# Kernel optimization log

Hardware: AMD Instinct MI355X
Metric: run time of the kernel (lower is better)

The kernel has to match this reference:

```python
import jax, jax.numpy as jnp
import numpy as np

N = 50000
E = 800000
IN_C = 128
OUT_C = 64
NEG_SLOPE = 0.2


def setup_inputs() -> dict:
    key = jax.random.key(0)
    k1, k2, k3, k4, k5 = jax.random.split(key, 5)
    x = jax.random.normal(k1, (N, IN_C), dtype=jnp.float32)
    edge_index = jax.random.randint(k2, (2, E), 0, N, dtype=jnp.int64)
    # GATv2Conv params (heads=1): lin_l (source), lin_r (target), att, bias
    sc_in = 1.0 / np.sqrt(IN_C)
    sc_out = 1.0 / np.sqrt(OUT_C)
    W_l = jax.random.normal(k3, (IN_C, OUT_C), dtype=jnp.float32) * sc_in
    W_r = jax.random.normal(k4, (IN_C, OUT_C), dtype=jnp.float32) * sc_in
    att = jax.random.normal(k5, (OUT_C,), dtype=jnp.float32) * sc_out
    bias = jnp.zeros((OUT_C,), dtype=jnp.float32)
    return {"x": x, "edge_index": edge_index, "W_l": W_l, "W_r": W_r,
            "att": att, "bias": bias}


def _gatv2(x, edge_index, W_l, W_r, att, bias):
    n = x.shape[0]
    # add self loops (PyG default add_self_loops=True)
    loop = jnp.arange(n, dtype=edge_index.dtype)
    src = jnp.concatenate([edge_index[0], loop])
    dst = jnpp_concat = jnp.concatenate([edge_index[1], loop])
    x_l = x @ W_l  # source transform [N, C]
    x_r = x @ W_r  # target transform [N, C]
    x_j = x_l[src]                      # [E+N, C] gathered source msgs
    e = jax.nn.leaky_relu(x_j + x_r[dst], NEG_SLOPE)
    logit = e @ att                     # [E+N]
    # segment softmax over edges grouped by destination node
    m = jax.ops.segment_max(logit, dst, num_segments=n)
    m = jnp.where(jnp.isfinite(m), m, 0.0)
    a = jnp.exp(logit - m[dst])
    denom = jax.ops.segment_sum(a, dst, num_segments=n)
    alpha = a / (denom[dst] + 1e-16)
    out = jax.ops.segment_sum(x_j * alpha[:, None], dst, num_segments=n)
    return out + bias


def reference(x, edge_index, W_l, W_r, att, bias):
    # dropout(p=0.6) is identity at inference
    h = jax.nn.elu(_gatv2(x, edge_index, W_l, W_r, att, bias))
    return jax.nn.log_softmax(h, axis=-1)
```

## Files before the change

kernel.cpp:

```cpp
#include <hip/hip_runtime.h>

#define N_NODES 50000
#define N_EDGES 800000
#define IN_C    128
#define OUT_C   64
#define NEG_SLOPE 0.2f

#define CAP     48

#define NB      196
#define NB_PAD  256
#define C_B     5120
#define EPB     4096
#define NP1     ((N_EDGES + EPB - 1) / EPB)
#define G_GEMM  ((N_NODES + 63) / 64)

#define GRID_MEGA 1024

typedef __bf16 bf16_8 __attribute__((ext_vector_type(8)));
typedef float  f32x4  __attribute__((ext_vector_type(4)));

__device__ __forceinline__ unsigned f2bf(float f) {
    unsigned u = __float_as_uint(f);
    return (u + 0x7fffu + ((u >> 16) & 1u)) >> 16;
}

__device__ __forceinline__ void wait_ge(int* ctr, int target) {
    int it = 0;
    while (__hip_atomic_load(ctr, __ATOMIC_ACQUIRE, __HIP_MEMORY_SCOPE_AGENT) < target) {
        __builtin_amdgcn_s_sleep(2);
        if (++it > (1 << 26)) break;
    }
}

__device__ __forceinline__ void grid_barrier(int* ctr, int nblk) {
    __syncthreads();
    if (threadIdx.x == 0) {
        __threadfence();
        __hip_atomic_fetch_add(ctr, 1, __ATOMIC_ACQ_REL, __HIP_MEMORY_SCOPE_AGENT);
        wait_ge(ctr, nblk);
        __threadfence();
    }
    __syncthreads();
}

__global__ __launch_bounds__(256) void k_prep(
    const float* __restrict__ Wl, const float* __restrict__ Wr,
    unsigned short* __restrict__ wtg, int* __restrict__ bcnt)
{
    int i = blockIdx.x * 256 + threadIdx.x;
    int k = i >> 6, cm = i & 63;
    if (k < 128) {
        wtg[(size_t)cm * 128 + k]        = (unsigned short)f2bf(Wl[(size_t)k * 64 + cm]);
        wtg[(size_t)(64 + cm) * 128 + k] = (unsigned short)f2bf(Wr[(size_t)k * 64 + cm]);
    }
    if (i < NB_PAD + 8) bcnt[i] = 0;
}

#define XPAD 136

__global__ __launch_bounds__(256, 4) void k_mega(
    const float* __restrict__ x, const unsigned short* __restrict__ wtg,
    const float* __restrict__ att, const int* __restrict__ ei,
    int* __restrict__ bcnt, unsigned* __restrict__ arena,
    unsigned short* __restrict__ xlb, unsigned short* __restrict__ xrb,
    float* __restrict__ qtil, int* __restrict__ cnt,
    unsigned short* __restrict__ csr_src, const float* __restrict__ bias,
    float* __restrict__ out)
{
    __shared__ __align__(16) char smem[25600];
    const int tid = threadIdx.x;
    const int b = (int)blockIdx.x;
    const int nblk = (int)gridDim.x;
    int* p1done = bcnt + NB_PAD;
    int* fullbar = bcnt + NB_PAD + 1;

    if (b < NP1) {
        unsigned* sorted = (unsigned*)smem;
        int* bc     = (int*)(smem + 16384);
        int* bstart = (int*)(smem + 16384 + 1024);
        int* gbase  = (int*)(smem + 16384 + 2048);
        int* bofs   = (int*)(smem + 16384 + 3072);

        int e0 = b * EPB;
        int nE = N_EDGES - e0; if (nE > EPB) nE = EPB;

        unsigned pk[16]; int bk[16];
#pragma unroll
        for (int jj = 0; jj < 4; ++jj) {
            int rel = jj * 1024 + tid * 4;
            if (rel + 3 < nE) {
                int4 d4 = *(const int4*)(ei + N_EDGES + e0 + rel);
                int4 s4 = *(const int4*)(ei + e0 + rel);
                int d[4] = {d4.x, d4.y, d4.z, d4.w};
                int s[4] = {s4.x, s4.y, s4.z, s4.w};
#pragma unroll
                for (int k2 = 0; k2 < 4; ++k2) {
                    pk[jj*4+k2] = ((unsigned)d[k2] << 16) | (unsigned)s[k2];
                    bk[jj*4+k2] = d[k2] >> 8;
                }
            } else {
#pragma unroll
                for (int k2 = 0; k2 < 4; ++k2) {
                    int e = rel + k2;
                    if (e < nE) {
                        int d = ei[N_EDGES + e0 + e], s = ei[e0 + e];
                        pk[jj*4+k2] = ((unsigned)d << 16) | (unsigned)s;
                        bk[jj*4+k2] = d >> 8;
                    } else bk[jj*4+k2] = -1;
                }
            }
        }

        bc[tid] = 0;
        __syncthreads();
#pragma unroll
        for (int i = 0; i < 16; ++i)
            if (bk[i] >= 0) atomicAdd(&bc[bk[i]], 1);
        __syncthreads();
        if (tid < 64) {
            int c0 = bc[tid*4], c1 = bc[tid*4+1], c2 = bc[tid*4+2], c3 = bc[tid*4+3];
            int t0 = c0, t1 = t0 + c1, t2 = t1 + c2, t3 = t2 + c3;
            int incl = t3;
#pragma unroll
            for (int o = 1; o < 64; o <<= 1) {
                int v = __shfl_up(incl, o);
                if (tid >= o) incl += v;
            }
            int ex = incl - t3;
            bstart[tid*4]   = ex;
            bstart[tid*4+1] = ex + t0;
            bstart[tid*4+2] = ex + t1;
            bstart[tid*4+3] = ex + t2;
        }
        __syncthreads();
        {
            int c = bc[tid];
            bofs[tid] = bstart[tid];
            if (c > 0) gbase[tid] = atomicAdd(&bcnt[tid], c);
        }
        __syncthreads();
#pragma unroll
        for (int i = 0; i < 16; ++i)
            if (bk[i] >= 0) {
                int p = atomicAdd(&bofs[bk[i]], 1);
                sorted[p] = pk[i];
            }
        __syncthreads();
        for (int p = tid; p < nE; p += 256) {
            unsigned v = sorted[p];
            int b2 = v >> 24;
            int gg = gbase[b2] + (p - bstart[b2]);
            if (gg < C_B) arena[(size_t)b2 * C_B + gg] = v;
        }

        __syncthreads();
        if (tid == 0) {
            __threadfence();
            __hip_atomic_fetch_add(p1done, 1, __ATOMIC_ACQ_REL, __HIP_MEMORY_SCOPE_AGENT);
            wait_ge(p1done, NP1);
            __threadfence();
        }
        __syncthreads();

        unsigned short* lcsr = (unsigned short*)smem;
        int* lcnt = (int*)(smem + 24576);
        const int n0 = b << 8;
        int nloc = N_NODES - n0; if (nloc > 256) nloc = 256;

        lcnt[tid] = 0;
        __syncthreads();

        int ne = bcnt[b]; if (ne > C_B) ne = C_B;
        const unsigned* ap = arena + (size_t)b * C_B;
        for (int p = tid; p < ne; p += 256) {
            unsigned v = ap[p];
            int dl  = (v >> 16) & 255;
            int pos = atomicAdd(&lcnt[dl], 1);
            if (pos < CAP) lcsr[dl * CAP + pos] = (unsigned short)(v & 0xffffu);
        }
        __syncthreads();

        if (tid < nloc) {
            int pos = lcnt[tid];
            if (pos < CAP) lcsr[tid * CAP + pos] = (unsigned short)(n0 + tid);
            cnt[n0 + tid] = pos + 1;
        }
        __syncthreads();

        const uint4* ls = (const uint4*)lcsr;
        uint4* gd = (uint4*)(csr_src + (size_t)n0 * CAP);
        int nv = nloc * 6;
        for (int i = tid; i < nv; i += 256) gd[i] = ls[i];
    } else if (b < NP1 + G_GEMM) {
        unsigned short* xs = (unsigned short*)smem;
        const int nbase = (b - NP1) * 64;

        const float4* x4 = (const float4*)x;
        for (int i = tid; i < 2048; i += 256) {
            int row = i >> 5, qq = i & 31;
            int node = nbase + row;
            float4 v = make_float4(0.f, 0.f, 0.f, 0.f);
            if (node < N_NODES) v = x4[(size_t)node * 32 + qq];
            uint2 p;
            p.x = f2bf(v.x) | (f2bf(v.y) << 16);
            p.y = f2bf(v.z) | (f2bf(v.w) << 16);
            *(uint2*)&xs[row * XPAD + qq * 4] = p;
        }
        __syncthreads();

        const int lane = tid & 63, wave = tid >> 6;
        const int m = lane & 15, quad = lane >> 4;

        bf16_8 af[4];
#pragma unroll
        for (int kt = 0; kt < 4; ++kt)
            af[kt] = *(const bf16_8*)&xs[(wave * 16 + m) * XPAD + kt * 32 + quad * 8];

        f32x4 accs[4];
#pragma unroll
        for (int t = 0; t < 4; ++t) {
            f32x4 acc = {0.f, 0.f, 0.f, 0.f};
#pragma unroll
            for (int kt = 0; kt < 4; ++kt) {
                bf16_8 bfr = *(const bf16_8*)&wtg[(size_t)(t * 16 + m) * 128 + kt * 32 + quad * 8];
                acc = __builtin_amdgcn_mfma_f32_16x16x32_bf16(af[kt], bfr, acc, 0, 0, 0);
            }
            accs[t] = acc;
#pragma unroll
            for (int r = 0; r < 4; ++r) {
                int node = nbase + wave * 16 + quad * 4 + r;
                if (node < N_NODES)
                    xlb[(size_t)node * 64 + t * 16 + m] = (unsigned short)f2bf(acc[r]);
            }
        }
        {
            float am[4];
#pragma unroll
            for (int t = 0; t < 4; ++t) am[t] = 0.6f * att[t * 16 + m];
            float part[4];
#pragma unroll
            for (int r = 0; r < 4; ++r) {
                part[r] = am[0] * accs[0][r];
#pragma unroll
                for (int t = 1; t < 4; ++t) part[r] = fmaf(am[t], accs[t][r], part[r]);
            }
#pragma unroll
            for (int o = 1; o <= 8; o <<= 1)
#pragma unroll
                for (int r = 0; r < 4; ++r) part[r] += __shfl_xor(part[r], o);
            if (m == 0) {
#pragma unroll
                for (int r = 0; r < 4; ++r) {
                    int node = nbase + wave * 16 + quad * 4 + r;
                    if (node < N_NODES) qtil[node] = part[r];
                }
            }
        }
#pragma unroll
        for (int t = 4; t < 8; ++t) {
            f32x4 acc = {0.f, 0.f, 0.f, 0.f};
#pragma unroll
            for (int kt = 0; kt < 4; ++kt) {
                bf16_8 bfr = *(const bf16_8*)&wtg[(size_t)(t * 16 + m) * 128 + kt * 32 + quad * 8];
                acc = __builtin_amdgcn_mfma_f32_16x16x32_bf16(af[kt], bfr, acc, 0, 0, 0);
            }
            int col = t * 16 + m - 64;
#pragma unroll
            for (int r = 0; r < 4; ++r) {
                int node = nbase + wave * 16 + quad * 4 + r;
                if (node < N_NODES)
                    xrb[(size_t)node * 64 + col] = (unsigned short)f2bf(acc[r]);
            }
        }
    }

    grid_barrier(fullbar, nblk);

    const unsigned lane = tid & 63;
    const unsigned g = lane >> 3;
    const unsigned q = lane & 7;
    const int wave = tid >> 6;
    const int wstride = nblk * 4;

    const uint4* xl4 = (const uint4*)xlb;

    const float4* atp = (const float4*)(att + q * 8);
    float4 ata = atp[0], atb = atp[1];
    float atv[8] = {ata.x, ata.y, ata.z, ata.w, atb.x, atb.y, atb.z, atb.w};
#pragma unroll
    for (int j = 0; j < 8; ++j) atv[j] *= 0.4f;
    const float4* bp = (const float4*)(bias + q * 8);
    float4 ba = bp[0], bb = bp[1];
    float bv[8] = {ba.x, ba.y, ba.z, ba.w, bb.x, bb.y, bb.z, bb.w};

    for (int wid = b * 4 + wave; wid < N_NODES; wid += wstride) {
        const unsigned short* cs = csr_src + (unsigned)wid * CAP;

        uint4 XR = ((const uint4*)xrb)[(unsigned)wid * 8 + q];
        float xrv[8];
        xrv[0] = __uint_as_float(XR.x << 16); xrv[1] = __uint_as_float(XR.x & 0xffff0000u);
        xrv[2] = __uint_as_float(XR.y << 16); xrv[3] = __uint_as_float(XR.y & 0xffff0000u);
        xrv[4] = __uint_as_float(XR.z << 16); xrv[5] = __uint_as_float(XR.z & 0xffff0000u);
        xrv[6] = __uint_as_float(XR.w << 16); xrv[7] = __uint_as_float(XR.w & 0xffff0000u);

        int deg = cnt[wid];
        if (deg > CAP) deg = CAP;
        int iters = (deg + 7) >> 3;

        float s = 0.f;
        float acc[8] = {0.f, 0.f, 0.f, 0.f, 0.f, 0.f, 0.f, 0.f};

        int e = (int)g;
        bool va = e < deg;
        unsigned sA = va ? (unsigned)cs[e] : (unsigned)wid;
        uint4 A = xl4[(sA << 3) + q];
        float QA = qtil[sA];
        e += 8;
        bool vb = e < deg;
        unsigned sB = vb ? (unsigned)cs[e] : (unsigned)wid;
        uint4 B = xl4[(sB << 3) + q];
        float QB = qtil[sB];

        for (int it = 0; it < iters; ++it) {
            uint4 C = A; float QC = QA; bool vc = va;
            A = B; QA = QB; va = vb;
            e += 8;
            vb = e < deg;
            unsigned sN = vb ? (unsigned)cs[e] : (unsigned)wid;
            B = xl4[(sN << 3) + q];
            QB = qtil[sN];

            float c[8];
            c[0] = __uint_as_float(C.x << 16);
            c[1] = __uint_as_float(C.x & 0xffff0000u);
            c[2] = __uint_as_float(C.y << 16);
            c[3] = __uint_as_float(C.y & 0xffff0000u);
            c[4] = __uint_as_float(C.z << 16);
            c[5] = __uint_as_float(C.z & 0xffff0000u);
            c[6] = __uint_as_float(C.w << 16);
            c[7] = __uint_as_float(C.w & 0xffff0000u);

            float r = 0.f;
#pragma unroll
            for (int j = 0; j < 8; ++j) {
                float t = c[j] + xrv[j];
                r = fmaf(atv[j], fabsf(t), r);
            }
            r += __shfl_xor(r, 1);
            r += __shfl_xor(r, 2);
            r += __shfl_xor(r, 4);

            float w = vc ? __expf(QC + r) : 0.f;
            s += w;
#pragma unroll
            for (int j = 0; j < 8; ++j) acc[j] = fmaf(w, c[j], acc[j]);
        }

#pragma unroll
        for (int o = 8; o <= 32; o <<= 1) {
            s += __shfl_xor(s, o);
#pragma unroll
            for (int j = 0; j < 8; ++j) acc[j] += __shfl_xor(acc[j], o);
        }

        float inv = 1.f / (s + 1e-16f);
        float h[8];
        float mx = -INFINITY;
#pragma unroll
        for (int j = 0; j < 8; ++j) {
            float hh = fmaf(acc[j], inv, bv[j]);
            hh = (hh > 0.f) ? hh : (__expf(hh) - 1.f);
            h[j] = hh;
            mx = fmaxf(mx, hh);
        }
#pragma unroll
        for (int o = 1; o <= 4; o <<= 1) mx = fmaxf(mx, __shfl_xor(mx, o));
        float ex = 0.f;
#pragma unroll
        for (int j = 0; j < 8; ++j) ex += __expf(h[j] - mx);
#pragma unroll
        for (int o = 1; o <= 4; o <<= 1) ex += __shfl_xor(ex, o);
        float lse = mx + __logf(ex);

        if (g == 0) {
            float4* op = (float4*)(out + (unsigned)wid * 64 + q * 8);
            op[0] = make_float4(h[0] - lse, h[1] - lse, h[2] - lse, h[3] - lse);
            op[1] = make_float4(h[4] - lse, h[5] - lse, h[6] - lse, h[7] - lse);
        }
    }
}

__global__ __launch_bounds__(256) void k_gemm_p1(
    const float* __restrict__ x, const unsigned short* __restrict__ wtg,
    const float* __restrict__ att, const int* __restrict__ ei,
    int* __restrict__ bcnt, unsigned* __restrict__ arena,
    unsigned short* __restrict__ xlb, unsigned short* __restrict__ xrb,
    float* __restrict__ qtil)
{
    __shared__ __align__(16) char smem[20480];
    const int tid = threadIdx.x;

    if (blockIdx.x >= G_GEMM) {
        unsigned* sorted = (unsigned*)smem;
        int* bc     = (int*)(smem + 16384);
        int* bstart = (int*)(smem + 16384 + 1024);
        int* gbase  = (int*)(smem + 16384 + 2048);
        int* bofs   = (int*)(smem + 16384 + 3072);

        int bid = blockIdx.x - G_GEMM;
        int e0 = bid * EPB;
        int nE = N_EDGES - e0; if (nE > EPB) nE = EPB;

        unsigned pk[16]; int bk[16];
#pragma unroll
        for (int jj = 0; jj < 4; ++jj) {
            int rel = jj * 1024 + tid * 4;
            if (rel + 3 < nE) {
                int4 d4 = *(const int4*)(ei + N_EDGES + e0 + rel);
                int4 s4 = *(const int4*)(ei + e0 + rel);
                int d[4] = {d4.x, d4.y, d4.z, d4.w};
                int s[4] = {s4.x, s4.y, s4.z, s4.w};
#pragma unroll
                for (int k2 = 0; k2 < 4; ++k2) {
                    pk[jj*4+k2] = ((unsigned)d[k2] << 16) | (unsigned)s[k2];
                    bk[jj*4+k2] = d[k2] >> 8;
                }
            } else {
#pragma unroll
                for (int k2 = 0; k2 < 4; ++k2) {
                    int e = rel + k2;
                    if (e < nE) {
                        int d = ei[N_EDGES + e0 + e], s = ei[e0 + e];
                        pk[jj*4+k2] = ((unsigned)d << 16) | (unsigned)s;
                        bk[jj*4+k2] = d >> 8;
                    } else bk[jj*4+k2] = -1;
                }
            }
        }

        bc[tid] = 0;
        __syncthreads();
#pragma unroll
        for (int i = 0; i < 16; ++i)
            if (bk[i] >= 0) atomicAdd(&bc[bk[i]], 1);
        __syncthreads();
        if (tid < 64) {
            int c0 = bc[tid*4], c1 = bc[tid*4+1], c2 = bc[tid*4+2], c3 = bc[tid*4+3];
            int t0 = c0, t1 = t0 + c1, t2 = t1 + c2, t3 = t2 + c3;
            int incl = t3;
#pragma unroll
            for (int o = 1; o < 64; o <<= 1) {
                int v = __shfl_up(incl, o);
                if (tid >= o) incl += v;
            }
            int ex = incl - t3;
            bstart[tid*4]   = ex;
            bstart[tid*4+1] = ex + t0;
            bstart[tid*4+2] = ex + t1;
            bstart[tid*4+3] = ex + t2;
        }
        __syncthreads();
        {
            int c = bc[tid];
            bofs[tid] = bstart[tid];
            if (c > 0) gbase[tid] = atomicAdd(&bcnt[tid], c);
        }
        __syncthreads();
#pragma unroll
        for (int i = 0; i < 16; ++i)
            if (bk[i] >= 0) {
                int p = atomicAdd(&bofs[bk[i]], 1);
                sorted[p] = pk[i];
            }
        __syncthreads();
        for (int p = tid; p < nE; p += 256) {
            unsigned v = sorted[p];
            int b2 = v >> 24;
            int gg = gbase[b2] + (p - bstart[b2]);
            if (gg < C_B) arena[(size_t)b2 * C_B + gg] = v;
        }
        return;
    }

    unsigned short* xs = (unsigned short*)smem;
    const int nbase = blockIdx.x * 64;

    const float4* x4 = (const float4*)x;
    for (int i = tid; i < 2048; i += 256) {
        int row = i >> 5, qq = i & 31;
        int node = nbase + row;
        float4 v = make_float4(0.f, 0.f, 0.f, 0.f);
        if (node < N_NODES) v = x4[(size_t)node * 32 + qq];
        uint2 p;
        p.x = f2bf(v.x) | (f2bf(v.y) << 16);
        p.y = f2bf(v.z) | (f2bf(v.w) << 16);
        *(uint2*)&xs[row * XPAD + qq * 4] = p;
    }
    __syncthreads();

    const int lane = tid & 63, wave = tid >> 6;
    const int m = lane & 15, quad = lane >> 4;

    bf16_8 af[4];
#pragma unroll
    for (int kt = 0; kt < 4; ++kt)
        af[kt] = *(const bf16_8*)&xs[(wave * 16 + m) * XPAD + kt * 32 + quad * 8];

    f32x4 accs[4];
#pragma unroll
    for (int t = 0; t < 4; ++t) {
        f32x4 acc = {0.f, 0.f, 0.f, 0.f};
#pragma unroll
        for (int kt = 0; kt < 4; ++kt) {
            bf16_8 bfr = *(const bf16_8*)&wtg[(size_t)(t * 16 + m) * 128 + kt * 32 + quad * 8];
            acc = __builtin_amdgcn_mfma_f32_16x16x32_bf16(af[kt], bfr, acc, 0, 0, 0);
        }
        accs[t] = acc;
#pragma unroll
        for (int r = 0; r < 4; ++r) {
            int node = nbase + wave * 16 + quad * 4 + r;
            if (node < N_NODES)
                xlb[(size_t)node * 64 + t * 16 + m] = (unsigned short)f2bf(acc[r]);
        }
    }
    {
        float am[4];
#pragma unroll
        for (int t = 0; t < 4; ++t) am[t] = 0.6f * att[t * 16 + m];
        float part[4];
#pragma unroll
        for (int r = 0; r < 4; ++r) {
            part[r] = am[0] * accs[0][r];
#pragma unroll
            for (int t = 1; t < 4; ++t) part[r] = fmaf(am[t], accs[t][r], part[r]);
        }
#pragma unroll
        for (int o = 1; o <= 8; o <<= 1)
#pragma unroll
            for (int r = 0; r < 4; ++r) part[r] += __shfl_xor(part[r], o);
        if (m == 0) {
#pragma unroll
            for (int r = 0; r < 4; ++r) {
                int node = nbase + wave * 16 + quad * 4 + r;
                if (node < N_NODES) qtil[node] = part[r];
            }
        }
    }
#pragma unroll
    for (int t = 4; t < 8; ++t) {
        f32x4 acc = {0.f, 0.f, 0.f, 0.f};
#pragma unroll
        for (int kt = 0; kt < 4; ++kt) {
            bf16_8 bfr = *(const bf16_8*)&wtg[(size_t)(t * 16 + m) * 128 + kt * 32 + quad * 8];
            acc = __builtin_amdgcn_mfma_f32_16x16x32_bf16(af[kt], bfr, acc, 0, 0, 0);
        }
        int col = t * 16 + m - 64;
#pragma unroll
        for (int r = 0; r < 4; ++r) {
            int node = nbase + wave * 16 + quad * 4 + r;
            if (node < N_NODES)
                xrb[(size_t)node * 64 + col] = (unsigned short)f2bf(acc[r]);
        }
    }
}

__global__ __launch_bounds__(256) void k_csr(
    const unsigned* __restrict__ arena, const int* __restrict__ bcnt,
    int* __restrict__ cnt, unsigned short* __restrict__ csr_src)
{
    __shared__ __align__(16) unsigned short lcsr[256 * CAP];
    __shared__ int lcnt[256];
    const int b = blockIdx.x, tid = threadIdx.x;
    const int n0 = b << 8;
    int nloc = N_NODES - n0; if (nloc > 256) nloc = 256;

    lcnt[tid] = 0;
    __syncthreads();

    int ne = bcnt[b]; if (ne > C_B) ne = C_B;
    const unsigned* ap = arena + (size_t)b * C_B;
    for (int p = tid; p < ne; p += 256) {
        unsigned v = ap[p];
        int dl  = (v >> 16) & 255;
        int pos = atomicAdd(&lcnt[dl], 1);
        if (pos < CAP) lcsr[dl * CAP + pos] = (unsigned short)(v & 0xffffu);
    }
    __syncthreads();

    if (tid < nloc) {
        int pos = lcnt[tid];
        if (pos < CAP) lcsr[tid * CAP + pos] = (unsigned short)(n0 + tid);
        cnt[n0 + tid] = pos + 1;
    }
    __syncthreads();

    const uint4* ls = (const uint4*)lcsr;
    uint4* gd = (uint4*)(csr_src + (size_t)n0 * CAP);
    int nv = nloc * 6;
    for (int i = tid; i < nv; i += 256) gd[i] = ls[i];
}

__global__ __launch_bounds__(256) void k_fused(
    const int* __restrict__ cnt, const unsigned short* __restrict__ csr_src,
    const unsigned short* __restrict__ xlb, const unsigned short* __restrict__ xrb,
    const float* __restrict__ qtil, const float* __restrict__ att,
    const float* __restrict__ bias, float* __restrict__ out)
{
    int wid  = (blockIdx.x * 256 + threadIdx.x) >> 6;
    if (wid >= N_NODES) return;
    unsigned lane = threadIdx.x & 63;
    unsigned g = lane >> 3;
    unsigned q = lane & 7;

    const uint4* xl4 = (const uint4*)xlb;
    const unsigned short* cs = csr_src + (unsigned)wid * CAP;

    uint4 XR = ((const uint4*)xrb)[(unsigned)wid * 8 + q];
    float xrv[8];
    xrv[0] = __uint_as_float(XR.x << 16); xrv[1] = __uint_as_float(XR.x & 0xffff0000u);
    xrv[2] = __uint_as_float(XR.y << 16); xrv[3] = __uint_as_float(XR.y & 0xffff0000u);
    xrv[4] = __uint_as_float(XR.z << 16); xrv[5] = __uint_as_float(XR.z & 0xffff0000u);
    xrv[6] = __uint_as_float(XR.w << 16); xrv[7] = __uint_as_float(XR.w & 0xffff0000u);

    const float4* atp = (const float4*)(att + q * 8);
    float4 ata = atp[0], atb = atp[1];
    float atv[8] = {ata.x, ata.y, ata.z, ata.w, atb.x, atb.y, atb.z, atb.w};
#pragma unroll
    for (int j = 0; j < 8; ++j) atv[j] *= 0.4f;

    int deg = cnt[wid];
    if (deg > CAP) deg = CAP;
    int iters = (deg + 7) >> 3;

    float s = 0.f;
    float acc[8] = {0.f, 0.f, 0.f, 0.f, 0.f, 0.f, 0.f, 0.f};

    int e = (int)g;
    bool va = e < deg;
    unsigned sA = va ? (unsigned)cs[e] : (unsigned)wid;
    uint4 A = xl4[(sA << 3) + q];
    float QA = qtil[sA];
    e += 8;
    bool vb = e < deg;
    unsigned sB = vb ? (unsigned)cs[e] : (unsigned)wid;
    uint4 B = xl4[(sB << 3) + q];
    float QB = qtil[sB];

    for (int it = 0; it < iters; ++it) {
        uint4 C = A; float QC = QA; bool vc = va;
        A = B; QA = QB; va = vb;
        e += 8;
        vb = e < deg;
        unsigned sN = vb ? (unsigned)cs[e] : (unsigned)wid;
        B = xl4[(sN << 3) + q];
        QB = qtil[sN];

        float c[8];
        c[0] = __uint_as_float(C.x << 16);
        c[1] = __uint_as_float(C.x & 0xffff0000u);
        c[2] = __uint_as_float(C.y << 16);
        c[3] = __uint_as_float(C.y & 0xffff0000u);
        c[4] = __uint_as_float(C.z << 16);
        c[5] = __uint_as_float(C.z & 0xffff0000u);
        c[6] = __uint_as_float(C.w << 16);
        c[7] = __uint_as_float(C.w & 0xffff0000u);

        float r = 0.f;
#pragma unroll
        for (int j = 0; j < 8; ++j) {
            float t = c[j] + xrv[j];
            r = fmaf(atv[j], fabsf(t), r);
        }
        r += __shfl_xor(r, 1);
        r += __shfl_xor(r, 2);
        r += __shfl_xor(r, 4);

        float w = vc ? __expf(QC + r) : 0.f;
        s += w;
#pragma unroll
        for (int j = 0; j < 8; ++j) acc[j] = fmaf(w, c[j], acc[j]);
    }

#pragma unroll
    for (int o = 8; o <= 32; o <<= 1) {
        s += __shfl_xor(s, o);
#pragma unroll
        for (int j = 0; j < 8; ++j) acc[j] += __shfl_xor(acc[j], o);
    }

    float inv = 1.f / (s + 1e-16f);
    const float4* bp = (const float4*)(bias + q * 8);
    float4 ba = bp[0], bb = bp[1];
    float bv[8] = {ba.x, ba.y, ba.z, ba.w, bb.x, bb.y, bb.z, bb.w};
    float h[8];
    float mx = -INFINITY;
#pragma unroll
    for (int j = 0; j < 8; ++j) {
        float hh = fmaf(acc[j], inv, bv[j]);
        hh = (hh > 0.f) ? hh : (__expf(hh) - 1.f);
        h[j] = hh;
        mx = fmaxf(mx, hh);
    }
#pragma unroll
    for (int o = 1; o <= 4; o <<= 1) mx = fmaxf(mx, __shfl_xor(mx, o));
    float ex = 0.f;
#pragma unroll
    for (int j = 0; j < 8; ++j) ex += __expf(h[j] - mx);
#pragma unroll
    for (int o = 1; o <= 4; o <<= 1) ex += __shfl_xor(ex, o);
    float lse = mx + __logf(ex);

    if (g == 0) {
        float4* op = (float4*)(out + (unsigned)wid * 64 + q * 8);
        op[0] = make_float4(h[0] - lse, h[1] - lse, h[2] - lse, h[3] - lse);
        op[1] = make_float4(h[4] - lse, h[5] - lse, h[6] - lse, h[7] - lse);
    }
}

extern "C" void kernel_launch(void* const* d_in, const int* in_sizes, int n_in,
                              void* d_out, int out_size, void* d_ws, size_t ws_size,
                              hipStream_t stream)
{
    const float* x    = (const float*)d_in[0];
    const int*   ei   = (const int*)  d_in[1];
    const float* Wl   = (const float*)d_in[2];
    const float* Wr   = (const float*)d_in[3];
    const float* att  = (const float*)d_in[4];
    const float* bias = (const float*)d_in[5];
    float* out = (float*)d_out;

    char* w = (char*)d_ws;
    unsigned short* xlb = (unsigned short*)w; w += (size_t)N_NODES * 64 * 2;
    unsigned short* xrb = (unsigned short*)w; w += (size_t)N_NODES * 64 * 2;
    unsigned short* csr_src = (unsigned short*)w; w += (size_t)N_NODES * CAP * 2;
    int*   cnt     = (int*)w;    w += (size_t)N_NODES * 4;
    float* qtil    = (float*)w;  w += (size_t)N_NODES * 4;
    unsigned short* wtg = (unsigned short*)w; w += (size_t)128 * 128 * 2;
    unsigned* arena = (unsigned*)w; w += (size_t)NB * C_B * 4;
    int* bcnt = (int*)w; w += (size_t)(NB_PAD + 8) * 4;

    static int mode = -1;
    if (mode < 0) {
        int nb = 0;
        hipError_t err = hipOccupancyMaxActiveBlocksPerMultiprocessor(
            &nb, reinterpret_cast<const void*>(k_mega), 256, 0);
        mode = (err == hipSuccess && nb >= 4) ? 1 : 0;
    }

    k_prep<<<32, 256, 0, stream>>>(Wl, Wr, wtg, bcnt);

    if (mode == 1) {
        k_mega<<<GRID_MEGA, 256, 0, stream>>>(
            x, wtg, att, ei, bcnt, arena, xlb, xrb, qtil, cnt, csr_src, bias, out);
    } else {
        k_gemm_p1<<<G_GEMM + NP1, 256, 0, stream>>>(
            x, wtg, att, ei, bcnt, arena, xlb, xrb, qtil);
        k_csr<<<NB, 256, 0, stream>>>(arena, bcnt, cnt, csr_src);
        k_fused<<<(N_NODES * 64 + 255) / 256, 256, 0, stream>>>(
            cnt, csr_src, xlb, xrb, qtil, att, bias, out);
    }
}
```

Measured before the change: 143.7 us.

## Split persistent mega kernel at grid barrier into build kernel plus separate aggregation launch

Removes the software grid barrier and the persistent aggregation phase from the mega kernel. The build kernel now does only CSR construction and the GEMM, launched with exactly NP1+G_GEMM blocks. Aggregation runs in the existing k_fused kernel as a separate launch. This trades the cost of the spin-wait barrier, and the persistent grid limited by occupancy, for an extra kernel launch boundary.

```diff
diff --git a/kernel.cpp b/kernel.cpp
--- a/kernel.cpp
+++ b/kernel.cpp
@@ -14,8 +14,7 @@
 #define EPB     4096
 #define NP1     ((N_EDGES + EPB - 1) / EPB)
 #define G_GEMM  ((N_NODES + 63) / 64)
-
-#define GRID_MEGA 1024
+#define G_BUILD (NP1 + G_GEMM)
 
 typedef __bf16 bf16_8 __attribute__((ext_vector_type(8)));
 typedef float  f32x4  __attribute__((ext_vector_type(4)));
@@ -31,17 +30,6 @@
         __builtin_amdgcn_s_sleep(2);
         if (++it > (1 << 26)) break;
     }
-}
-
-__device__ __forceinline__ void grid_barrier(int* ctr, int nblk) {
-    __syncthreads();
-    if (threadIdx.x == 0) {
-        __threadfence();
-        __hip_atomic_fetch_add(ctr, 1, __ATOMIC_ACQ_REL, __HIP_MEMORY_SCOPE_AGENT);
-        wait_ge(ctr, nblk);
-        __threadfence();
-    }
-    __syncthreads();
 }
 
 __global__ __launch_bounds__(256) void k_prep(
@@ -59,21 +47,18 @@
 
 #define XPAD 136
 
-__global__ __launch_bounds__(256, 4) void k_mega(
+__global__ __launch_bounds__(256, 4) void k_build(
     const float* __restrict__ x, const unsigned short* __restrict__ wtg,
     const float* __restrict__ att, const int* __restrict__ ei,
     int* __restrict__ bcnt, unsigned* __restrict__ arena,
     unsigned short* __restrict__ xlb, unsigned short* __restrict__ xrb,
     float* __restrict__ qtil, int* __restrict__ cnt,
-    unsigned short* __restrict__ csr_src, const float* __restrict__ bias,
-    float* __restrict__ out)
+    unsigned short* __restrict__ csr_src)
 {
     __shared__ __align__(16) char smem[25600];
     const int tid = threadIdx.x;
     const int b = (int)blockIdx.x;
-    const int nblk = (int)gridDim.x;
     int* p1done = bcnt + NB_PAD;
-    int* fullbar = bcnt + NB_PAD + 1;
 
     if (b < NP1) {
         unsigned* sorted = (unsigned*)smem;
@@ -192,7 +177,7 @@
         uint4* gd = (uint4*)(csr_src + (size_t)n0 * CAP);
         int nv = nloc * 6;
         for (int i = tid; i < nv; i += 256) gd[i] = ls[i];
-    } else if (b < NP1 + G_GEMM) {
+    } else {
         unsigned short* xs = (unsigned short*)smem;
         const int nbase = (b - NP1) * 64;
 
@@ -272,121 +257,6 @@
                 if (node < N_NODES)
                     xrb[(size_t)node * 64 + col] = (unsigned short)f2bf(acc[r]);
             }
-        }
-    }
-
-    grid_barrier(fullbar, nblk);
-
-    const unsigned lane = tid & 63;
-    const unsigned g = lane >> 3;
-    const unsigned q = lane & 7;
-    const int wave = tid >> 6;
-    const int wstride = nblk * 4;
-
-    const uint4* xl4 = (const uint4*)xlb;
-
-    const float4* atp = (const float4*)(att + q * 8);
-    float4 ata = atp[0], atb = atp[1];
-    float atv[8] = {ata.x, ata.y, ata.z, ata.w, atb.x, atb.y, atb.z, atb.w};
-#pragma unroll
-    for (int j = 0; j < 8; ++j) atv[j] *= 0.4f;
-    const float4* bp = (const float4*)(bias + q * 8);
-    float4 ba = bp[0], bb = bp[1];
-    float bv[8] = {ba.x, ba.y, ba.z, ba.w, bb.x, bb.y, bb.z, bb.w};
-
-    for (int wid = b * 4 + wave; wid < N_NODES; wid += wstride) {
-        const unsigned short* cs = csr_src + (unsigned)wid * CAP;
-
-        uint4 XR = ((const uint4*)xrb)[(unsigned)wid * 8 + q];
-        float xrv[8];
-        xrv[0] = __uint_as_float(XR.x << 16); xrv[1] = __uint_as_float(XR.x & 0xffff0000u);
-        xrv[2] = __uint_as_float(XR.y << 16); xrv[3] = __uint_as_float(XR.y & 0xffff0000u);
-        xrv[4] = __uint_as_float(XR.z << 16); xrv[5] = __uint_as_float(XR.z & 0xffff0000u);
-        xrv[6] = __uint_as_float(XR.w << 16); xrv[7] = __uint_as_float(XR.w & 0xffff0000u);
-
-        int deg = cnt[wid];
-        if (deg > CAP) deg = CAP;
-        int iters = (deg + 7) >> 3;
-
-        float s = 0.f;
-        float acc[8] = {0.f, 0.f, 0.f, 0.f, 0.f, 0.f, 0.f, 0.f};
-
-        int e = (int)g;
-        bool va = e < deg;
-        unsigned sA = va ? (unsigned)cs[e] : (unsigned)wid;
-        uint4 A = xl4[(sA << 3) + q];
-        float QA = qtil[sA];
-        e += 8;
-        bool vb = e < deg;
-        unsigned sB = vb ? (unsigned)cs[e] : (unsigned)wid;
-        uint4 B = xl4[(sB << 3) + q];
-        float QB = qtil[sB];
-
-        for (int it = 0; it < iters; ++it) {
-            uint4 C = A; float QC = QA; bool vc = va;
-            A = B; QA = QB; va = vb;
-            e += 8;
-            vb = e < deg;
-            unsigned sN = vb ? (unsigned)cs[e] : (unsigned)wid;
-            B = xl4[(sN << 3) + q];
-            QB = qtil[sN];
-
-            float c[8];
-            c[0] = __uint_as_float(C.x << 16);
-            c[1] = __uint_as_float(C.x & 0xffff0000u);
-            c[2] = __uint_as_float(C.y << 16);
-            c[3] = __uint_as_float(C.y & 0xffff0000u);
-            c[4] = __uint_as_float(C.z << 16);
-            c[5] = __uint_as_float(C.z & 0xffff0000u);
-            c[6] = __uint_as_float(C.w << 16);
-            c[7] = __uint_as_float(C.w & 0xffff0000u);
-
-            float r = 0.f;
-#pragma unroll
-            for (int j = 0; j < 8; ++j) {
-                float t = c[j] + xrv[j];
-                r = fmaf(atv[j], fabsf(t), r);
-            }
-            r += __shfl_xor(r, 1);
-            r += __shfl_xor(r, 2);
-            r += __shfl_xor(r, 4);
-
-            float w = vc ? __expf(QC + r) : 0.f;
-            s += w;
-#pragma unroll
-            for (int j = 0; j < 8; ++j) acc[j] = fmaf(w, c[j], acc[j]);
-        }
-
-#pragma unroll
-        for (int o = 8; o <= 32; o <<= 1) {
-            s += __shfl_xor(s, o);
-#pragma unroll
-            for (int j = 0; j < 8; ++j) acc[j] += __shfl_xor(acc[j], o);
-        }
-
-        float inv = 1.f / (s + 1e-16f);
-        float h[8];
-        float mx = -INFINITY;
-#pragma unroll
-        for (int j = 0; j < 8; ++j) {
-            float hh = fmaf(acc[j], inv, bv[j]);
-            hh = (hh > 0.f) ? hh : (__expf(hh) - 1.f);
-            h[j] = hh;
-            mx = fmaxf(mx, hh);
-        }
-#pragma unroll
-        for (int o = 1; o <= 4; o <<= 1) mx = fmaxf(mx, __shfl_xor(mx, o));
-        float ex = 0.f;
-#pragma unroll
-        for (int j = 0; j < 8; ++j) ex += __expf(h[j] - mx);
-#pragma unroll
-        for (int o = 1; o <= 4; o <<= 1) ex += __shfl_xor(ex, o);
-        float lse = mx + __logf(ex);
-
-        if (g == 0) {
-            float4* op = (float4*)(out + (unsigned)wid * 64 + q * 8);
-            op[0] = make_float4(h[0] - lse, h[1] - lse, h[2] - lse, h[3] - lse);
-            op[1] = make_float4(h[4] - lse, h[5] - lse, h[6] - lse, h[7] - lse);
         }
     }
 }
@@ -744,20 +614,20 @@
     if (mode < 0) {
         int nb = 0;
         hipError_t err = hipOccupancyMaxActiveBlocksPerMultiprocessor(
-            &nb, reinterpret_cast<const void*>(k_mega), 256, 0);
+            &nb, reinterpret_cast<const void*>(k_build), 256, 0);
         mode = (err == hipSuccess && nb >= 4) ? 1 : 0;
     }
 
     k_prep<<<32, 256, 0, stream>>>(Wl, Wr, wtg, bcnt);
 
     if (mode == 1) {
-        k_mega<<<GRID_MEGA, 256, 0, stream>>>(
-            x, wtg, att, ei, bcnt, arena, xlb, xrb, qtil, cnt, csr_src, bias, out);
+        k_build<<<G_BUILD, 256, 0, stream>>>(
+            x, wtg, att, ei, bcnt, arena, xlb, xrb, qtil, cnt, csr_src);
     } else {
         k_gemm_p1<<<G_GEMM + NP1, 256, 0, stream>>>(
             x, wtg, att, ei, bcnt, arena, xlb, xrb, qtil);
         k_csr<<<NB, 256, 0, stream>>>(arena, bcnt, cnt, csr_src);
-        k_fused<<<(N_NODES * 64 + 255) / 256, 256, 0, stream>>>(
-            cnt, csr_src, xlb, xrb, qtil, att, bias, out);
-    }
-}
+    }
+    k_fused<<<(N_NODES * 64 + 255) / 256, 256, 0, stream>>>(
+        cnt, csr_src, xlb, xrb, qtil, att, bias, out);
+}
```

New measurement: 165.5 us. 15.1% more time.
